# Performance work log

Hardware: AMD Instinct MI355X
Metric: run time of the kernel (lower is better)

Reference implementation:

```python
import jax, jax.numpy as jnp
import numpy as np

E = 8            # num_local_experts
K = 2            # top-2 gate
CAP_FACTOR = 1.0 # tutel default capacity factor


def setup_inputs() -> dict:
    key = jax.random.key(0)
    k0, k1, k2, k3 = jax.random.split(key, 4)
    B, N, D, H = 8, 8192, 512, 512
    s = 0.02
    return {
        "x": jax.random.normal(k0, (B, N, D), jnp.float32),
        "Wg": jax.random.normal(k1, (D, E), jnp.float32) * s,
        "W1": jax.random.normal(k2, (E, D, H), jnp.float32) * s,
        "b1": jnp.zeros((E, H), jnp.float32),
        "W2": jax.random.normal(k3, (E, H, D), jnp.float32) * s,
        "b2": jnp.zeros((E, D), jnp.float32),
    }


def _moe(x, Wg, W1, b1, W2, b2):
    B, N, D = x.shape
    T = B * N
    xt = x.reshape(T, D)
    # --- gating (Top2Gate): softmax over experts, take top-2, renormalize ---
    gates = jax.nn.softmax(xt @ Wg, axis=-1)            # [T, E]
    topw, topi = jax.lax.top_k(gates, K)                # [T, K]
    topw = topw / jnp.sum(topw, axis=-1, keepdims=True)
    # --- capacity & per-expert positions (k=0 assignments fill first) ---
    C = int(np.ceil(K * T / E * CAP_FACTOR))
    onehot = jax.nn.one_hot(topi, E, dtype=jnp.int32)   # [T, K, E]
    flat = onehot.transpose(1, 0, 2).reshape(K * T, E)  # k-major order
    pos_flat = jnp.cumsum(flat, axis=0) - 1             # running count per expert
    pos = (pos_flat * flat).sum(-1).reshape(K, T).T     # [T, K] slot within expert
    keep = (pos < C).astype(xt.dtype)                   # [T, K] capacity drop mask
    # --- dispatch: scatter tokens into [E, C, D] expert buffers ---
    ei = topi.reshape(-1)                               # [T*K]
    pi = jnp.clip(pos, 0, C - 1).reshape(-1)            # [T*K]
    vals = (xt[:, None, :] * keep[:, :, None]).reshape(T * K, D)
    buf = jnp.zeros((E, C, D), xt.dtype).at[ei, pi].add(vals)
    # --- per-expert FFN (identity activation) ---
    h = jnp.einsum('ecd,edh->ech', buf, W1) + b1[:, None, :]
    out = jnp.einsum('ech,ehd->ecd', h, W2) + b2[:, None, :]
    # --- combine: gather expert outputs, weight, sum over k ---
    gathered = out[ei, pi].reshape(T, K, D)
    y = jnp.sum(gathered * (topw * keep)[:, :, None], axis=1)
    return y.reshape(B, N, D)


def reference(x, Wg, W1, b1, W2, b2):
    y = _moe(x, Wg, W1, b1, W2, b2)        # [B, N, D]
    return jax.nn.log_softmax(jnp.sum(y, axis=2), axis=1)  # [B, N]
```

## Files before the change

### kernel.cpp

```cpp
#include <hip/hip_runtime.h>

#define T_TOK 65536
#define DDIM 512
#define NEXP 8
#define CAP 16384

__device__ inline float wave_sum(float v) {
#pragma unroll
  for (int m = 1; m < 64; m <<= 1) v += __shfl_xor(v, m, 64);
  return v;
}

template <int CTRL>
__device__ __forceinline__ float dppf(float v) {
  return __int_as_float(
      __builtin_amdgcn_mov_dpp(__float_as_int(v), CTRL, 0xf, 0xf, true));
}
__device__ __forceinline__ void pl32swap(float& a, float& b) {
  asm("v_permlane32_swap_b32 %0, %1" : "+v"(a), "+v"(b));
}
__device__ __forceinline__ void pl16swap(float& a, float& b) {
  asm("v_permlane16_swap_b32 %0, %1" : "+v"(a), "+v"(b));
}

__global__ void k_w2s(const float* __restrict__ W2, const float* __restrict__ Wg,
                      float* __restrict__ w2s, float* __restrict__ wT) {
  if (blockIdx.x < 1024) {
    int w = threadIdx.x >> 6, lane = threadIdx.x & 63;
    int row = blockIdx.x * 4 + w;
    const float* p = W2 + (size_t)row * 512;
    float sum = 0.f;
#pragma unroll
    for (int j = 0; j < 8; ++j) sum += p[lane + j * 64];
    sum = wave_sum(sum);
    if (lane == 0) w2s[row] = sum;
  } else {
    int i = (blockIdx.x - 1024) * 256 + threadIdx.x;
    int e = i >> 9, d = i & 511;
    wT[i] = Wg[d * 8 + e];
  }
}

__global__ void k_v_beta(const float* __restrict__ W1, const float* __restrict__ b1,
                         const float* __restrict__ b2, const float* __restrict__ w2s,
                         float* __restrict__ wT, float* __restrict__ beta) {
  int w = threadIdx.x >> 6, lane = threadIdx.x & 63;
  if (blockIdx.x < 1024) {
    int rid = blockIdx.x * 4 + w;
    int e = rid >> 9, d = rid & 511;
    const float* p = W1 + (size_t)rid * 512;
    const float* q = w2s + e * 512;
    float sum = 0.f;
#pragma unroll
    for (int j = 0; j < 8; ++j) { int h = lane + j * 64; sum += p[h] * q[h]; }
    sum = wave_sum(sum);
    if (lane == 0) wT[(size_t)(8 + e) * 512 + d] = sum;
  } else {
#pragma unroll
    for (int r = 0; r < 2; ++r) {
      int e = w + r * 4;
      float sum = 0.f;
#pragma unroll
      for (int j = 0; j < 8; ++j) {
        int i = lane + j * 64;
        sum += b1[e * 512 + i] * w2s[e * 512 + i] + b2[e * 512 + i];
      }
      sum = wave_sum(sum);
      if (lane == 0) beta[e] = sum;
    }
  }
}

__global__ __launch_bounds__(1024, 4) void k_dots(const float* __restrict__ x,
                                                  const float* __restrict__ wT,
                                                  const float* __restrict__ beta,
                                                  float4* __restrict__ wd,
                                                  int* __restrict__ epk,
                                                  int* __restrict__ hist) {
  __shared__ float sD[256 * 17];
  __shared__ int c0[8], c1[8];
  const int tid = threadIdx.x;
  const int lane = tid & 63;
  const int wave = tid >> 6;
  const int wo = wave & 1;
  const int tset = wave >> 1;
  const int tbase = blockIdx.x * 256 + tset * 32;

  float w[8][8];
#pragma unroll
  for (int o = 0; o < 8; ++o) {
    const float* wp = wT + (size_t)(wo * 8 + o) * 512 + 8 * lane;
    float4 wa = *reinterpret_cast<const float4*>(wp);
    float4 wb = *reinterpret_cast<const float4*>(wp + 4);
    w[o][0] = wa.x; w[o][1] = wa.y; w[o][2] = wa.z; w[o][3] = wa.w;
    w[o][4] = wb.x; w[o][5] = wb.y; w[o][6] = wb.z; w[o][7] = wb.w;
  }

  const bool kb3 = (lane & 8) != 0;
  const float* xb = x + (size_t)tbase * 512 + 8 * lane;

  auto proc = [&](int r, float4 x0, float4 x1) {
    float p[8];
#pragma unroll
    for (int o = 0; o < 8; ++o)
      p[o] = x0.x * w[o][0] + x0.y * w[o][1] + x0.z * w[o][2] + x0.w * w[o][3] +
             x1.x * w[o][4] + x1.y * w[o][5] + x1.z * w[o][6] + x1.w * w[o][7];
    float a[4];
#pragma unroll
    for (int j = 0; j < 4; ++j) {
      float u = p[j], v = p[j + 4];
      pl32swap(u, v);
      a[j] = u + v;
    }
    float b[2];
#pragma unroll
    for (int j = 0; j < 2; ++j) {
      float u = a[j], v = a[j + 2];
      pl16swap(u, v);
      b[j] = u + v;
    }
    float snd = kb3 ? b[0] : b[1];
    float kp  = kb3 ? b[1] : b[0];
    float c = kp + dppf<0x128>(snd);
    c += dppf<0x141>(c);
    c += dppf<0x4E>(c);
    c += dppf<0xB1>(c);
    if ((lane & 7) == 0)
      sD[(tset * 32 + r) * 17 + wo * 8 + (lane >> 3)] = c;
  };

  float4 s00, s01, s10, s11, s20, s21, s30, s31;
  const float* q;
  q = xb;        s00 = *reinterpret_cast<const float4*>(q); s01 = *reinterpret_cast<const float4*>(q + 4);
  q = xb + 512;  s10 = *reinterpret_cast<const float4*>(q); s11 = *reinterpret_cast<const float4*>(q + 4);
  q = xb + 1024; s20 = *reinterpret_cast<const float4*>(q); s21 = *reinterpret_cast<const float4*>(q + 4);

#pragma unroll
  for (int r = 0; r < 32; r += 4) {
    q = xb + (size_t)(r + 3) * 512;
    s30 = *reinterpret_cast<const float4*>(q); s31 = *reinterpret_cast<const float4*>(q + 4);
    proc(r, s00, s01);
    if (r + 4 < 32) {
      q = xb + (size_t)(r + 4) * 512;
      s00 = *reinterpret_cast<const float4*>(q); s01 = *reinterpret_cast<const float4*>(q + 4);
    }
    proc(r + 1, s10, s11);
    if (r + 5 < 32) {
      q = xb + (size_t)(r + 5) * 512;
      s10 = *reinterpret_cast<const float4*>(q); s11 = *reinterpret_cast<const float4*>(q + 4);
    }
    proc(r + 2, s20, s21);
    if (r + 6 < 32) {
      q = xb + (size_t)(r + 6) * 512;
      s20 = *reinterpret_cast<const float4*>(q); s21 = *reinterpret_cast<const float4*>(q + 4);
    }
    proc(r + 3, s30, s31);
  }

  __syncthreads();
  if (tid < 8) { c0[tid] = 0; c1[tid] = 0; }
  __syncthreads();
  if (tid < 256) {
    const int t = blockIdx.x * 256 + tid;
    float l[8], dv[8];
#pragma unroll
    for (int e = 0; e < 8; ++e) { l[e] = sD[tid * 17 + e]; dv[e] = sD[tid * 17 + 8 + e]; }
    int e1 = 0; float v1 = l[0];
#pragma unroll
    for (int e = 1; e < 8; ++e) if (l[e] > v1) { v1 = l[e]; e1 = e; }
    int e2 = 0; float v2 = -3.4e38f;
#pragma unroll
    for (int e = 0; e < 8; ++e) if (e != e1 && l[e] > v2) { v2 = l[e]; e2 = e; }
    float wexp = expf(v2 - v1);
    float w1 = 1.f / (1.f + wexp);
    float w2 = wexp * w1;
    float d1 = 0.f, d2 = 0.f;
#pragma unroll
    for (int e = 0; e < 8; ++e) {
      d1 = (e == e1) ? dv[e] : d1;
      d2 = (e == e2) ? dv[e] : d2;
    }
    float4 o; o.x = w1; o.y = w2; o.z = d1 + beta[e1]; o.w = d2 + beta[e2];
    wd[t] = o;
    epk[t] = e1 | (e2 << 8);
    atomicAdd(&c0[e1], 1);
    atomicAdd(&c1[e2], 1);
  }
  __syncthreads();
  if (tid < 8) {
    hist[blockIdx.x * 8 + tid] = c0[tid];
    hist[(256 + blockIdx.x) * 8 + tid] = c1[tid];
  }
}

__global__ __launch_bounds__(256) void k_keep(const int* __restrict__ hist,
                                              const int* __restrict__ epk,
                                              const float4* __restrict__ wd,
                                              float* __restrict__ s) {
  __shared__ int sA[256], sB[256];
  __shared__ int sOff0[8], sOff1[8];
  __shared__ int sC0[32], sC1[32];
  const int tid = threadIdx.x;
  const int b = blockIdx.x;

  {
    int e = tid & 7, c = tid >> 3;
    int v0 = 0, v1 = 0;
#pragma unroll
    for (int j = 0; j < 8; ++j) {
      int row = c * 8 + j;
      int h0 = hist[row * 8 + e];
      int h1 = hist[(256 + row) * 8 + e];
      if (row < b) v0 += h0;
      v1 += h0;
      if (row < b) v1 += h1;
    }
    sA[c * 8 + e] = v0;
    sB[c * 8 + e] = v1;
  }
  __syncthreads();
  if (tid < 8) {
    int t0 = 0, t1 = 0;
#pragma unroll
    for (int c = 0; c < 32; ++c) { t0 += sA[c * 8 + tid]; t1 += sB[c * 8 + tid]; }
    sOff0[tid] = t0;
    sOff1[tid] = t1;
  }
  __syncthreads();

  int lane = tid & 63, w = tid >> 6;
  int t = b * 256 + tid;
  int ep = epk[t]; int e1 = ep & 255, e2 = ep >> 8;
  unsigned long long lt = (1ull << lane) - 1ull;
  int wr0 = 0, wr1 = 0;
#pragma unroll
  for (int e = 0; e < 8; ++e) {
    unsigned long long m0 = __ballot(e1 == e);
    unsigned long long m1 = __ballot(e2 == e);
    if (e == e1) wr0 = __popcll(m0 & lt);
    if (e == e2) wr1 = __popcll(m1 & lt);
    if (lane == 0) { sC0[w * 8 + e] = __popcll(m0); sC1[w * 8 + e] = __popcll(m1); }
  }
  __syncthreads();
  int woff0 = 0, woff1 = 0;
  for (int wp = 0; wp < 4; ++wp) {
    if (wp < w) { woff0 += sC0[wp * 8 + e1]; woff1 += sC1[wp * 8 + e2]; }
  }
  int pos0 = sOff0[e1] + woff0 + wr0;
  int pos1 = sOff1[e2] + woff1 + wr1;
  float4 v = wd[t];
  float sv = 0.f;
  if (pos0 < CAP) sv += v.x * v.z;
  if (pos1 < CAP) sv += v.y * v.w;
  s[t] = sv;
}

__global__ __launch_bounds__(1024) void k_lsm(const float* __restrict__ s,
                                              float* __restrict__ out) {
  __shared__ float sRa[16], sRb[16];
  int tid = threadIdx.x, lane = tid & 63, w = tid >> 6;
  size_t base = (size_t)blockIdx.x * 8192;
  float v[8];
#pragma unroll
  for (int j = 0; j < 8; ++j) v[j] = s[base + tid + j * 1024];
  float mx = v[0];
#pragma unroll
  for (int j = 1; j < 8; ++j) mx = fmaxf(mx, v[j]);
#pragma unroll
  for (int m = 1; m < 64; m <<= 1) mx = fmaxf(mx, __shfl_xor(mx, m, 64));
  if (lane == 0) sRa[w] = mx;
  __syncthreads();
#pragma unroll
  for (int i = 0; i < 16; ++i) mx = fmaxf(mx, sRa[i]);
  float sum = 0.f;
#pragma unroll
  for (int j = 0; j < 8; ++j) sum += expf(v[j] - mx);
#pragma unroll
  for (int m = 1; m < 64; m <<= 1) sum += __shfl_xor(sum, m, 64);
  if (lane == 0) sRb[w] = sum;
  __syncthreads();
  float tot = 0.f;
#pragma unroll
  for (int i = 0; i < 16; ++i) tot += sRb[i];
  float lse = logf(tot);
#pragma unroll
  for (int j = 0; j < 8; ++j) out[base + tid + j * 1024] = v[j] - mx - lse;
}

extern "C" void kernel_launch(void* const* d_in, const int* in_sizes, int n_in,
                              void* d_out, int out_size, void* d_ws, size_t ws_size,
                              hipStream_t stream) {
  const float* x  = (const float*)d_in[0];
  const float* Wg = (const float*)d_in[1];
  const float* W1 = (const float*)d_in[2];
  const float* b1 = (const float*)d_in[3];
  const float* W2 = (const float*)d_in[4];
  const float* b2 = (const float*)d_in[5];
  float* out = (float*)d_out;
  char* ws = (char*)d_ws;

  float*  w2s  = (float*)(ws);
  float*  wT   = (float*)(ws + (16u << 10));
  float*  beta = (float*)(ws + (48u << 10));
  float4* wd   = (float4*)(ws + (64u << 10));
  int*    epk  = (int*)(ws + (64u << 10) + (1u << 20));
  int*    hist = (int*)(ws + (64u << 10) + (1u << 20) + (256u << 10));
  float*  s    = (float*)(ws + (64u << 10) + (1u << 20) + (288u << 10));

  hipLaunchKernelGGL(k_w2s,    dim3(1040), dim3(256),  0, stream, W2, Wg, w2s, wT);
  hipLaunchKernelGGL(k_v_beta, dim3(1025), dim3(256),  0, stream, W1, b1, b2, w2s, wT, beta);
  hipLaunchKernelGGL(k_dots,   dim3(256),  dim3(1024), 0, stream, x, wT, beta, wd, epk, hist);
  hipLaunchKernelGGL(k_keep,   dim3(256),  dim3(256),  0, stream, hist, epk, wd, s);
  hipLaunchKernelGGL(k_lsm,    dim3(8),    dim3(1024), 0, stream, s, out);
}
```

Measured before the change: 46.03 us.

## Split D across wave pairs in k_dots to halve weight registers

```diff
diff --git a/kernel.cpp b/kernel.cpp
--- a/kernel.cpp
+++ b/kernel.cpp
@@ -71,40 +71,36 @@
   }
 }
 
-__global__ __launch_bounds__(1024, 4) void k_dots(const float* __restrict__ x,
-                                                  const float* __restrict__ wT,
-                                                  const float* __restrict__ beta,
-                                                  float4* __restrict__ wd,
-                                                  int* __restrict__ epk,
-                                                  int* __restrict__ hist) {
-  __shared__ float sD[256 * 17];
+__global__ __launch_bounds__(512, 6) void k_dots(const float* __restrict__ x,
+                                                 const float* __restrict__ wT,
+                                                 const float* __restrict__ beta,
+                                                 float4* __restrict__ wd,
+                                                 int* __restrict__ epk,
+                                                 int* __restrict__ hist) {
+  __shared__ float sD[2][256 * 17];
   __shared__ int c0[8], c1[8];
   const int tid = threadIdx.x;
   const int lane = tid & 63;
   const int wave = tid >> 6;
   const int wo = wave & 1;
-  const int tset = wave >> 1;
-  const int tbase = blockIdx.x * 256 + tset * 32;
-
-  float w[8][8];
-#pragma unroll
-  for (int o = 0; o < 8; ++o) {
-    const float* wp = wT + (size_t)(wo * 8 + o) * 512 + 8 * lane;
-    float4 wa = *reinterpret_cast<const float4*>(wp);
-    float4 wb = *reinterpret_cast<const float4*>(wp + 4);
-    w[o][0] = wa.x; w[o][1] = wa.y; w[o][2] = wa.z; w[o][3] = wa.w;
-    w[o][4] = wb.x; w[o][5] = wb.y; w[o][6] = wb.z; w[o][7] = wb.w;
-  }
+  const int wp = (wave >> 1) & 1;
+  const int tset = wave >> 2;
+  const int tbase = blockIdx.x * 256 + tset * 128;
+
+  float4 w4[8];
+#pragma unroll
+  for (int o = 0; o < 8; ++o)
+    w4[o] = *reinterpret_cast<const float4*>(
+        wT + (size_t)(wo * 8 + o) * 512 + wp * 256 + 4 * lane);
 
   const bool kb3 = (lane & 8) != 0;
-  const float* xb = x + (size_t)tbase * 512 + 8 * lane;
-
-  auto proc = [&](int r, float4 x0, float4 x1) {
+  const float* xb = x + (size_t)tbase * 512 + wp * 256 + 4 * lane;
+
+  auto proc = [&](int r, float4 x0) {
     float p[8];
 #pragma unroll
     for (int o = 0; o < 8; ++o)
-      p[o] = x0.x * w[o][0] + x0.y * w[o][1] + x0.z * w[o][2] + x0.w * w[o][3] +
-             x1.x * w[o][4] + x1.y * w[o][5] + x1.z * w[o][6] + x1.w * w[o][7];
+      p[o] = x0.x * w4[o].x + x0.y * w4[o].y + x0.z * w4[o].z + x0.w * w4[o].w;
     float a[4];
 #pragma unroll
     for (int j = 0; j < 4; ++j) {
@@ -126,36 +122,22 @@
     c += dppf<0x4E>(c);
     c += dppf<0xB1>(c);
     if ((lane & 7) == 0)
-      sD[(tset * 32 + r) * 17 + wo * 8 + (lane >> 3)] = c;
+      sD[wp][(tset * 128 + r) * 17 + wo * 8 + (lane >> 3)] = c;
   };
 
-  float4 s00, s01, s10, s11, s20, s21, s30, s31;
-  const float* q;
-  q = xb;        s00 = *reinterpret_cast<const float4*>(q); s01 = *reinterpret_cast<const float4*>(q + 4);
-  q = xb + 512;  s10 = *reinterpret_cast<const float4*>(q); s11 = *reinterpret_cast<const float4*>(q + 4);
-  q = xb + 1024; s20 = *reinterpret_cast<const float4*>(q); s21 = *reinterpret_cast<const float4*>(q + 4);
-
-#pragma unroll
-  for (int r = 0; r < 32; r += 4) {
-    q = xb + (size_t)(r + 3) * 512;
-    s30 = *reinterpret_cast<const float4*>(q); s31 = *reinterpret_cast<const float4*>(q + 4);
-    proc(r, s00, s01);
-    if (r + 4 < 32) {
-      q = xb + (size_t)(r + 4) * 512;
-      s00 = *reinterpret_cast<const float4*>(q); s01 = *reinterpret_cast<const float4*>(q + 4);
-    }
-    proc(r + 1, s10, s11);
-    if (r + 5 < 32) {
-      q = xb + (size_t)(r + 5) * 512;
-      s10 = *reinterpret_cast<const float4*>(q); s11 = *reinterpret_cast<const float4*>(q + 4);
-    }
-    proc(r + 2, s20, s21);
-    if (r + 6 < 32) {
-      q = xb + (size_t)(r + 6) * 512;
-      s20 = *reinterpret_cast<const float4*>(q); s21 = *reinterpret_cast<const float4*>(q + 4);
-    }
-    proc(r + 3, s30, s31);
-  }
+#define LD(T) (*reinterpret_cast<const float4*>(xb + (size_t)(T) * 512))
+  float4 s0 = LD(0), s1 = LD(1), s2 = LD(2), s3;
+  for (int r = 0; r < 128; r += 4) {
+    s3 = LD(r + 3);
+    proc(r + 0, s0);
+    if (r + 4 < 128) s0 = LD(r + 4);
+    proc(r + 1, s1);
+    if (r + 5 < 128) s1 = LD(r + 5);
+    proc(r + 2, s2);
+    if (r + 6 < 128) s2 = LD(r + 6);
+    proc(r + 3, s3);
+  }
+#undef LD
 
   __syncthreads();
   if (tid < 8) { c0[tid] = 0; c1[tid] = 0; }
@@ -164,7 +146,10 @@
     const int t = blockIdx.x * 256 + tid;
     float l[8], dv[8];
 #pragma unroll
-    for (int e = 0; e < 8; ++e) { l[e] = sD[tid * 17 + e]; dv[e] = sD[tid * 17 + 8 + e]; }
+    for (int e = 0; e < 8; ++e) {
+      l[e]  = sD[0][tid * 17 + e]     + sD[1][tid * 17 + e];
+      dv[e] = sD[0][tid * 17 + 8 + e] + sD[1][tid * 17 + 8 + e];
+    }
     int e1 = 0; float v1 = l[0];
 #pragma unroll
     for (int e = 1; e < 8; ++e) if (l[e] > v1) { v1 = l[e]; e1 = e; }
@@ -309,7 +294,7 @@
 
   hipLaunchKernelGGL(k_w2s,    dim3(1040), dim3(256),  0, stream, W2, Wg, w2s, wT);
   hipLaunchKernelGGL(k_v_beta, dim3(1025), dim3(256),  0, stream, W1, b1, b2, w2s, wT, beta);
-  hipLaunchKernelGGL(k_dots,   dim3(256),  dim3(1024), 0, stream, x, wT, beta, wd, epk, hist);
+  hipLaunchKernelGGL(k_dots,   dim3(256),  dim3(512),  0, stream, x, wT, beta, wd, epk, hist);
   hipLaunchKernelGGL(k_keep,   dim3(256),  dim3(256),  0, stream, hist, epk, wd, s);
   hipLaunchKernelGGL(k_lsm,    dim3(8),    dim3(1024), 0, stream, s, out);
 }
```

Result: slower. 59.90 us (+30.2%).
